# Kernel optimization log

Measured on AMD Instinct MI355X. Metric: run time of the kernel, lower is better.

The kernel has to match this reference:

```python
import jax, jax.numpy as jnp
import numpy as np

B, S, H, F, E, K = 2, 2048, 1024, 4096, 8, 2
NH = H // 128  # heads of dim 128, per SimpleMoEBlock.__init__
DH = H // NH


def _layernorm(x, g, b, eps=1e-5):
    m = x.mean(-1, keepdims=True)
    v = ((x - m) ** 2).mean(-1, keepdims=True)
    return (x - m) / jnp.sqrt(v + eps) * g + b


def _forward(x, ln_attn_g, ln_attn_b, ln_mlp_g, ln_mlp_b,
             in_proj_w, in_proj_b, out_proj_w, out_proj_b,
             router_w, fc1_w, fc1_b, fc2_w, fc2_b):
    # --- self attention (nn.MultiheadAttention, batch_first, no mask) ---
    xa = _layernorm(x, ln_attn_g, ln_attn_b)                    # [B,S,H]
    qkv = xa @ in_proj_w.T + in_proj_b                          # [B,S,3H]
    q, k, v = jnp.split(qkv, 3, axis=-1)
    def heads(t):
        return t.reshape(B, S, NH, DH).transpose(0, 2, 1, 3)    # [B,NH,S,DH]
    q, k, v = heads(q), heads(k), heads(v)
    scores = jnp.einsum('bhqd,bhkd->bhqk', q, k) / jnp.sqrt(jnp.asarray(DH, x.dtype))
    attn = jnp.einsum('bhqk,bhkd->bhqd', jax.nn.softmax(scores, axis=-1), v)
    attn = attn.transpose(0, 2, 1, 3).reshape(B, S, H)
    attn = attn @ out_proj_w.T + out_proj_b
    h = x + attn                                                # residual

    # --- MoE feed-forward ---
    y = _layernorm(h, ln_mlp_g, ln_mlp_b).reshape(B * S, H)     # flat tokens [T,H]
    logits = y @ router_w.T                                     # [T,E]
    probs = jax.nn.softmax(logits, axis=-1)
    top_scores, top_idx = jax.lax.top_k(probs, K)               # [T,K]
    # per-token per-expert combine weight; 0 for unrouted tokens -> identical
    # math to torch's index_select/index_add dispatch
    w = (jax.nn.one_hot(top_idx, E, dtype=y.dtype) * top_scores[..., None]).sum(axis=1)  # [T,E]

    combined = jnp.zeros_like(y)
    for e in range(E):  # fixed small expert count
        he = jax.nn.silu(y @ fc1_w[e].T + fc1_b[e])             # [T,F]
        oe = he @ fc2_w[e].T + fc2_b[e]                         # [T,H]
        combined = combined + oe * w[:, e:e + 1]
    return h + combined.reshape(B, S, H)


def setup_inputs() -> dict:
    key = jax.random.key(0)
    ks = jax.random.split(key, 8)
    s = 0.02
    return {
        'x': jax.random.normal(ks[0], (B, S, H), jnp.float32),
        'ln_attn_g': jnp.ones((H,), jnp.float32),
        'ln_attn_b': jnp.zeros((H,), jnp.float32),
        'ln_mlp_g': jnp.ones((H,), jnp.float32),
        'ln_mlp_b': jnp.zeros((H,), jnp.float32),
        'in_proj_w': jax.random.normal(ks[1], (3 * H, H), jnp.float32) * s,
        'in_proj_b': jnp.zeros((3 * H,), jnp.float32),
        'out_proj_w': jax.random.normal(ks[2], (H, H), jnp.float32) * s,
        'out_proj_b': jnp.zeros((H,), jnp.float32),
        'router_w': jax.random.normal(ks[3], (E, H), jnp.float32) * s,
        'fc1_w': jax.random.normal(ks[4], (E, F, H), jnp.float32) * s,
        'fc1_b': jnp.zeros((E, F), jnp.float32),
        'fc2_w': jax.random.normal(ks[5], (E, H, F), jnp.float32) * s,
        'fc2_b': jnp.zeros((E, H), jnp.float32),
    }


def reference(x, ln_attn_g, ln_attn_b, ln_mlp_g, ln_mlp_b,
              in_proj_w, in_proj_b, out_proj_w, out_proj_b,
              router_w, fc1_w, fc1_b, fc2_w, fc2_b):
    return _forward(x, ln_attn_g, ln_attn_b, ln_mlp_g, ln_mlp_b,
                    in_proj_w, in_proj_b, out_proj_w, out_proj_b,
                    router_w, fc1_w, fc1_b, fc2_w, fc2_b)
```

## Files before the change

### kernel.cpp

```cpp
#include <hip/hip_runtime.h>

#define T_TOK 4096
#define S_SEQ 2048
#define H_DIM 1024
#define H3    3072
#define NHEAD 8
#define DHEAD 128
#define F_DIM 4096
#define NEXP  8
#define MAX_RB 72
#define NSLOT 9216

typedef __bf16 bf16x8 __attribute__((ext_vector_type(8)));
typedef float  f32x4  __attribute__((ext_vector_type(4)));
typedef __attribute__((address_space(1))) const unsigned int* gas1_t;
typedef __attribute__((address_space(3))) unsigned int* las3_t;

__device__ __forceinline__ unsigned short f2bf(float f){
  unsigned int u = __builtin_bit_cast(unsigned int, f);
  u += 0x7fffu + ((u>>16)&1u);
  return (unsigned short)(u>>16);
}
__device__ __forceinline__ float bf2f(unsigned short h){
  unsigned int u = ((unsigned int)h)<<16;
  return __builtin_bit_cast(float, u);
}
__device__ __forceinline__ f32x4 MF(bf16x8 a, bf16x8 b, f32x4 c){
  return __builtin_amdgcn_mfma_f32_16x16x32_bf16(a,b,c,0,0,0);
}
__device__ __forceinline__ void gload16(const void* g, void* l){
  __builtin_amdgcn_global_load_lds((gas1_t)g, (las3_t)l, 16, 0, 0);
}
__device__ __forceinline__ float blockReduceSum(float v){
  __shared__ float sh_red[4];
  #pragma unroll
  for(int o=32;o>0;o>>=1) v += __shfl_down(v,o,64);
  int w = threadIdx.x>>6;
  if((threadIdx.x&63)==0) sh_red[w]=v;
  __syncthreads();
  float tot = sh_red[0]+sh_red[1]+sh_red[2]+sh_red[3];
  __syncthreads();
  return tot;
}

__global__ __launch_bounds__(256) void k_ln_split(const float* __restrict__ x,
    const float* __restrict__ g, const float* __restrict__ bta,
    unsigned short* __restrict__ hi, unsigned short* __restrict__ lo){
  int t = blockIdx.x, tid = threadIdx.x;
  float4 v = reinterpret_cast<const float4*>(x + (size_t)t*H_DIM)[tid];
  float mean = blockReduceSum(v.x+v.y+v.z+v.w) * (1.0f/H_DIM);
  float d0=v.x-mean,d1=v.y-mean,d2=v.z-mean,d3=v.w-mean;
  float var = blockReduceSum(d0*d0+d1*d1+d2*d2+d3*d3) * (1.0f/H_DIM);
  float rstd = rsqrtf(var + 1e-5f);
  float4 gv = reinterpret_cast<const float4*>(g)[tid];
  float4 bv = reinterpret_cast<const float4*>(bta)[tid];
  float o0=d0*rstd*gv.x+bv.x, o1=d1*rstd*gv.y+bv.y, o2=d2*rstd*gv.z+bv.z, o3=d3*rstd*gv.w+bv.w;
  size_t base = (size_t)t*H_DIM + tid*4;
  unsigned short h0=f2bf(o0),h1=f2bf(o1),h2=f2bf(o2),h3=f2bf(o3);
  *reinterpret_cast<ushort4*>(hi+base) = make_ushort4(h0,h1,h2,h3);
  *reinterpret_cast<ushort4*>(lo+base) = make_ushort4(
      f2bf(o0-bf2f(h0)), f2bf(o1-bf2f(h1)), f2bf(o2-bf2f(h2)), f2bf(o3-bf2f(h3)));
}

__global__ __launch_bounds__(256) void k_wsplit(const float* __restrict__ w,
    unsigned short* __restrict__ hi, unsigned short* __restrict__ lo, int n4){
  int i = blockIdx.x*256 + threadIdx.x;
  if(i>=n4) return;
  float4 v = reinterpret_cast<const float4*>(w)[i];
  size_t base = (size_t)i*4;
  unsigned short h0=f2bf(v.x),h1=f2bf(v.y),h2=f2bf(v.z),h3=f2bf(v.w);
  *reinterpret_cast<ushort4*>(hi+base) = make_ushort4(h0,h1,h2,h3);
  *reinterpret_cast<ushort4*>(lo+base) = make_ushort4(
      f2bf(v.x-bf2f(h0)), f2bf(v.y-bf2f(h1)), f2bf(v.z-bf2f(h2)), f2bf(v.w-bf2f(h3)));
}

__global__ __launch_bounds__(256) void k_wconv(const float* __restrict__ w,
    unsigned short* __restrict__ hi, int n4){
  int i = blockIdx.x*256 + threadIdx.x;
  if(i>=n4) return;
  float4 v = reinterpret_cast<const float4*>(w)[i];
  *reinterpret_cast<ushort4*>(hi + (size_t)i*4) =
      make_ushort4(f2bf(v.x), f2bf(v.y), f2bf(v.z), f2bf(v.w));
}

template<int EPI>
__global__ __launch_bounds__(256) void k_gemm_split(
    const unsigned short* __restrict__ Ah, const unsigned short* __restrict__ Al,
    const unsigned short* __restrict__ Bh, const unsigned short* __restrict__ Bl,
    const float* __restrict__ bias, const float* __restrict__ resid,
    unsigned short* __restrict__ Chi, unsigned short* __restrict__ Clo,
    float* __restrict__ Cf, int N, int Kd){
  int m0 = blockIdx.y*128, n0 = blockIdx.x*128;
  int tid=threadIdx.x, wid=tid>>6, lane=tid&63, lr=lane&15, lg=lane>>4;
  int wr=wid>>1, wc=wid&1;
  __shared__ unsigned short tAh[4096], tAl[4096], tBh[4096], tBl[4096];
  f32x4 acc[4][4] = {};
  for(int k0=0;k0<Kd;k0+=32){
    #pragma unroll
    for(int i=0;i<2;i++){
      int p = i*256 + tid;
      int row = p>>2, pc = p&3;
      int lc = pc ^ ((row>>1)&3);
      size_t go = (size_t)row*Kd + k0 + lc*8;
      int lb = (i*256 + wid*64)*8;
      gload16(Ah + (size_t)m0*Kd + go, tAh + lb);
      gload16(Al + (size_t)m0*Kd + go, tAl + lb);
      gload16(Bh + (size_t)n0*Kd + go, tBh + lb);
      gload16(Bl + (size_t)n0*Kd + go, tBl + lb);
    }
    asm volatile("s_waitcnt vmcnt(0)" ::: "memory");
    __syncthreads();
    bf16x8 ah[4], al[4], bh[4], bl[4];
    #pragma unroll
    for(int q=0;q<4;q++){
      int ra = wr*64+q*16+lr;
      int ia = ra*32 + ((lg ^ ((ra>>1)&3))<<3);
      ah[q] = *reinterpret_cast<const bf16x8*>(&tAh[ia]);
      al[q] = *reinterpret_cast<const bf16x8*>(&tAl[ia]);
      int rb = wc*64+q*16+lr;
      int ib = rb*32 + ((lg ^ ((rb>>1)&3))<<3);
      bh[q] = *reinterpret_cast<const bf16x8*>(&tBh[ib]);
      bl[q] = *reinterpret_cast<const bf16x8*>(&tBl[ib]);
    }
    #pragma unroll
    for(int mf=0;mf<4;mf++)
      #pragma unroll
      for(int nf=0;nf<4;nf++){
        acc[mf][nf] = MF(ah[mf], bh[nf], acc[mf][nf]);
        acc[mf][nf] = MF(ah[mf], bl[nf], acc[mf][nf]);
        acc[mf][nf] = MF(al[mf], bh[nf], acc[mf][nf]);
      }
    __syncthreads();
  }
  #pragma unroll
  for(int mf=0;mf<4;mf++)
    #pragma unroll
    for(int nf=0;nf<4;nf++)
      #pragma unroll
      for(int r=0;r<4;r++){
        int row = m0 + wr*64 + mf*16 + lg*4 + r;
        int col = n0 + wc*64 + nf*16 + lr;
        float v = acc[mf][nf][r] + bias[col];
        size_t idx = (size_t)row*N + col;
        if(EPI==0){
          unsigned short hb = f2bf(v);
          Chi[idx]=hb; Clo[idx]=f2bf(v-bf2f(hb));
        } else {
          Cf[idx] = v + resid[idx];
        }
      }
}

__global__ __launch_bounds__(256) void k_vtrans(const unsigned short* __restrict__ qh,
    const unsigned short* __restrict__ ql,
    unsigned short* __restrict__ vth, unsigned short* __restrict__ vtl){
  int bh = blockIdx.z, d0 = blockIdx.y*32, s0 = blockIdx.x*32;
  int b = bh>>3, hh = bh&7;
  int tid=threadIdx.x;
  __shared__ unsigned short th[32][40], tl[32][40];
  int sr = tid>>3, dc = (tid&7)*4;
  size_t src = ((size_t)(b*S_SEQ + s0 + sr))*H3 + 2*H_DIM + hh*DHEAD + d0 + dc;
  *reinterpret_cast<ushort4*>(&th[sr][dc]) = *reinterpret_cast<const ushort4*>(qh+src);
  *reinterpret_cast<ushort4*>(&tl[sr][dc]) = *reinterpret_cast<const ushort4*>(ql+src);
  __syncthreads();
  int dr = tid>>3, sc = (tid&7)*4;
  size_t dst = ((size_t)(bh*DHEAD) + d0+dr)*S_SEQ + s0 + sc;
  *reinterpret_cast<ushort4*>(vth+dst) = make_ushort4(th[sc][dr],th[sc+1][dr],th[sc+2][dr],th[sc+3][dr]);
  *reinterpret_cast<ushort4*>(vtl+dst) = make_ushort4(tl[sc][dr],tl[sc+1][dr],tl[sc+2][dr],tl[sc+3][dr]);
}

__global__ __launch_bounds__(256,2) void k_attn(const unsigned short* __restrict__ qkv_hi,
    const unsigned short* __restrict__ qkv_lo,
    const unsigned short* __restrict__ vt_hi, const unsigned short* __restrict__ vt_lo,
    float* __restrict__ opb, float* __restrict__ mlb, int kv_span){
  const float SCALE = 0.08838834764831843f;
  int qb = blockIdx.x, bh = blockIdx.y, zz = blockIdx.z;
  int b = bh>>3, hh = bh&7;
  int kvbase = zz*kv_span, kvend = kvbase + kv_span;
  int tid=threadIdx.x, wid=tid>>6, lane=tid&63, lr=lane&15, lg=lane>>4;
  __shared__ unsigned short kh[4096], kl[4096], vh[4096], vl[4096];
  __shared__ unsigned short ph[4][1024], pl[4][1024];
  int row0 = qb*128 + wid*32;
  bf16x8 qh_[2][4], ql_[2][4];
  #pragma unroll
  for(int j=0;j<2;j++){
    size_t qbase = ((size_t)(b*S_SEQ) + row0 + j*16 + lr)*H3 + hh*DHEAD;
    #pragma unroll
    for(int kk=0;kk<4;kk++){
      qh_[j][kk] = *reinterpret_cast<const bf16x8*>(qkv_hi + qbase + kk*32 + lg*8);
      ql_[j][kk] = *reinterpret_cast<const bf16x8*>(qkv_lo + qbase + kk*32 + lg*8);
    }
  }
  f32x4 o_acc[2][8] = {};
  float mrun[2] = {-1e30f,-1e30f};
  float lrun[2] = {0.f,0.f};

  auto STAGE = [&](int kv0){
    #pragma unroll
    for(int i=0;i<2;i++){
      int p = i*256 + tid;
      int lb = (i*256 + wid*64)*8;
      {
        int krow = p>>4, pc = p&15;
        int lc = (pc&8)|((pc&7)^(krow&7));
        size_t go = ((size_t)(b*S_SEQ + kv0 + krow))*H3 + H_DIM + hh*DHEAD + lc*8;
        gload16(qkv_hi + go, &kh[lb]);
        gload16(qkv_lo + go, &kl[lb]);
      }
      {
        int vrow = p>>2, pc = p&3;
        int lc = pc ^ ((vrow>>1)&3);
        size_t gv = ((size_t)(bh*DHEAD) + vrow)*S_SEQ + kv0 + lc*8;
        gload16(vt_hi + gv, &vh[lb]);
        gload16(vt_lo + gv, &vl[lb]);
      }
    }
  };

  for(int kv0=kvbase; kv0<kvend; kv0+=32){
    STAGE(kv0);
    asm volatile("s_waitcnt vmcnt(0)" ::: "memory");
    __syncthreads();
    f32x4 s0[2] = {}, s1[2] = {};
    __builtin_amdgcn_s_setprio(1);
    #pragma unroll
    for(int kk=0;kk<4;kk++){
      int c = kk*4+lg;
      int phys = (c&8)|((c&7)^(lr&7));
      bf16x8 kah = *reinterpret_cast<const bf16x8*>(&kh[lr*128 + phys*8]);
      bf16x8 kal = *reinterpret_cast<const bf16x8*>(&kl[lr*128 + phys*8]);
      bf16x8 kbh = *reinterpret_cast<const bf16x8*>(&kh[(16+lr)*128 + phys*8]);
      bf16x8 kbl = *reinterpret_cast<const bf16x8*>(&kl[(16+lr)*128 + phys*8]);
      #pragma unroll
      for(int j=0;j<2;j++){
        s0[j] = MF(kah, qh_[j][kk], s0[j]);
        s0[j] = MF(kah, ql_[j][kk], s0[j]);
        s0[j] = MF(kal, qh_[j][kk], s0[j]);
        s1[j] = MF(kbh, qh_[j][kk], s1[j]);
        s1[j] = MF(kbh, ql_[j][kk], s1[j]);
        s1[j] = MF(kbl, qh_[j][kk], s1[j]);
      }
    }
    __builtin_amdgcn_s_setprio(0);
    float sc[2][8]; float mt[2];
    #pragma unroll
    for(int j=0;j<2;j++){
      #pragma unroll
      for(int r=0;r<4;r++){ sc[j][r] = s0[j][r]*SCALE; sc[j][4+r] = s1[j][r]*SCALE; }
      float m_ = fmaxf(fmaxf(fmaxf(sc[j][0],sc[j][1]),fmaxf(sc[j][2],sc[j][3])),
                       fmaxf(fmaxf(sc[j][4],sc[j][5]),fmaxf(sc[j][6],sc[j][7])));
      m_ = fmaxf(m_, __shfl_xor(m_,16,64));
      m_ = fmaxf(m_, __shfl_xor(m_,32,64));
      mt[j] = m_;
    }
    int skip = __all((mt[0] <= mrun[0]+8.0f) && (mt[1] <= mrun[1]+8.0f));
    if(!skip){
      #pragma unroll
      for(int j=0;j<2;j++){
        float mn = fmaxf(mrun[j], mt[j]);
        float rs = __expf(mrun[j]-mn);
        lrun[j] *= rs; mrun[j] = mn;
        #pragma unroll
        for(int nf2=0;nf2<8;nf2++){
          f32x4 t = o_acc[j][nf2];
          t[0]*=rs; t[1]*=rs; t[2]*=rs; t[3]*=rs;
          o_acc[j][nf2] = t;
        }
      }
    }
    #pragma unroll
    for(int j=0;j<2;j++){
      float ssum = 0.f;
      #pragma unroll
      for(int i=0;i<8;i++){ sc[j][i] = __expf(sc[j][i]-mrun[j]); ssum += sc[j][i]; }
      ssum += __shfl_xor(ssum,16,64);
      ssum += __shfl_xor(ssum,32,64);
      lrun[j] += ssum;
      unsigned short hbk[8], lbk[8];
      #pragma unroll
      for(int i=0;i<8;i++){ hbk[i]=f2bf(sc[j][i]); lbk[i]=f2bf(sc[j][i]-bf2f(hbk[i])); }
      int half = (lg&1)*4;
      int a0 = j*512 + lr*32 + (((lg>>1)^(lr&3))<<3) + half;
      int a1 = j*512 + lr*32 + ((((lg>>1)+2)^(lr&3))<<3) + half;
      *reinterpret_cast<ushort4*>(&ph[wid][a0]) = make_ushort4(hbk[0],hbk[1],hbk[2],hbk[3]);
      *reinterpret_cast<ushort4*>(&pl[wid][a0]) = make_ushort4(lbk[0],lbk[1],lbk[2],lbk[3]);
      *reinterpret_cast<ushort4*>(&ph[wid][a1]) = make_ushort4(hbk[4],hbk[5],hbk[6],hbk[7]);
      *reinterpret_cast<ushort4*>(&pl[wid][a1]) = make_ushort4(lbk[4],lbk[5],lbk[6],lbk[7]);
    }
    bf16x8 pbh[2], pbl[2];
    #pragma unroll
    for(int j=0;j<2;j++){
      int pp = (lg^(lr&3))<<3;
      pbh[j] = *reinterpret_cast<const bf16x8*>(&ph[wid][j*512 + lr*32 + pp]);
      pbl[j] = *reinterpret_cast<const bf16x8*>(&pl[wid][j*512 + lr*32 + pp]);
    }
    __builtin_amdgcn_s_setprio(1);
    #pragma unroll
    for(int nf2=0;nf2<8;nf2++){
      int d = nf2*16 + lr;
      int vp = (lg ^ ((d>>1)&3))<<3;
      bf16x8 vah = *reinterpret_cast<const bf16x8*>(&vh[d*32 + vp]);
      bf16x8 val = *reinterpret_cast<const bf16x8*>(&vl[d*32 + vp]);
      #pragma unroll
      for(int j=0;j<2;j++){
        o_acc[j][nf2] = MF(vah, pbh[j], o_acc[j][nf2]);
        o_acc[j][nf2] = MF(vah, pbl[j], o_acc[j][nf2]);
        o_acc[j][nf2] = MF(val, pbh[j], o_acc[j][nf2]);
      }
    }
    __builtin_amdgcn_s_setprio(0);
    __syncthreads();
  }
  #pragma unroll
  for(int j=0;j<2;j++){
    int srow = row0 + j*16 + lr;
    size_t obase = (((size_t)zz*16 + bh)*S_SEQ + srow)*(size_t)DHEAD;
    #pragma unroll
    for(int nf2=0;nf2<8;nf2++){
      *reinterpret_cast<f32x4*>(&opb[obase + nf2*16 + lg*4]) = o_acc[j][nf2];
    }
    if(lg==0){
      *reinterpret_cast<float2*>(&mlb[(((size_t)zz*16 + bh)*S_SEQ + srow)*2]) =
          make_float2(mrun[j], lrun[j]);
    }
  }
}

__global__ __launch_bounds__(256) void k_amerge(const float* __restrict__ opb,
    const float* __restrict__ mlb, int nz,
    unsigned short* __restrict__ o_hi, unsigned short* __restrict__ o_lo){
  int bh = blockIdx.y, b = bh>>3, hh = bh&7;
  int r = threadIdx.x>>4;
  int c = (threadIdx.x&15)*8;
  int srow = blockIdx.x*16 + r;
  float mz[2], lz[2];
  float m = -1e30f;
  for(int z=0;z<nz;z++){
    const float* mlp = mlb + (((size_t)z*16 + bh)*S_SEQ + srow)*2;
    mz[z]=mlp[0]; lz[z]=mlp[1];
    m = fmaxf(m, mz[z]);
  }
  float L = 0.f, w[2];
  for(int z=0;z<nz;z++){ w[z] = __expf(mz[z]-m); L += lz[z]*w[z]; }
  float linv = 1.0f/L;
  float acc[8] = {0,0,0,0,0,0,0,0};
  for(int z=0;z<nz;z++){
    const float* o = opb + (((size_t)z*16 + bh)*S_SEQ + srow)*(size_t)DHEAD + c;
    float4 a = *reinterpret_cast<const float4*>(o);
    float4 bq = *reinterpret_cast<const float4*>(o+4);
    acc[0]+=a.x*w[z]; acc[1]+=a.y*w[z]; acc[2]+=a.z*w[z]; acc[3]+=a.w*w[z];
    acc[4]+=bq.x*w[z]; acc[5]+=bq.y*w[z]; acc[6]+=bq.z*w[z]; acc[7]+=bq.w*w[z];
  }
  size_t idx = ((size_t)(b*S_SEQ)+srow)*H_DIM + hh*DHEAD + c;
  unsigned short hp[8], lp[8];
  #pragma unroll
  for(int i=0;i<8;i++){
    float v = acc[i]*linv;
    hp[i]=f2bf(v); lp[i]=f2bf(v-bf2f(hp[i]));
  }
  *reinterpret_cast<ushort4*>(o_hi+idx)   = make_ushort4(hp[0],hp[1],hp[2],hp[3]);
  *reinterpret_cast<ushort4*>(o_hi+idx+4) = make_ushort4(hp[4],hp[5],hp[6],hp[7]);
  *reinterpret_cast<ushort4*>(o_lo+idx)   = make_ushort4(lp[0],lp[1],lp[2],lp[3]);
  *reinterpret_cast<ushort4*>(o_lo+idx+4) = make_ushort4(lp[4],lp[5],lp[6],lp[7]);
}

__global__ __launch_bounds__(256) void k_ln2_router(const float* __restrict__ h,
    const float* __restrict__ g, const float* __restrict__ bt, const float* __restrict__ rw,
    unsigned short* __restrict__ ybf, int* __restrict__ route_e, float* __restrict__ route_w){
  int t = blockIdx.x, tid = threadIdx.x;
  float4 v = reinterpret_cast<const float4*>(h + (size_t)t*H_DIM)[tid];
  float mean = blockReduceSum(v.x+v.y+v.z+v.w) * (1.0f/H_DIM);
  float d0=v.x-mean,d1=v.y-mean,d2=v.z-mean,d3=v.w-mean;
  float var = blockReduceSum(d0*d0+d1*d1+d2*d2+d3*d3) * (1.0f/H_DIM);
  float rstd = rsqrtf(var + 1e-5f);
  float4 gv = reinterpret_cast<const float4*>(g)[tid];
  float4 bv = reinterpret_cast<const float4*>(bt)[tid];
  float o0=d0*rstd*gv.x+bv.x, o1=d1*rstd*gv.y+bv.y, o2=d2*rstd*gv.z+bv.z, o3=d3*rstd*gv.w+bv.w;
  size_t base = (size_t)t*H_DIM + tid*4;
  *reinterpret_cast<ushort4*>(ybf+base) = make_ushort4(f2bf(o0),f2bf(o1),f2bf(o2),f2bf(o3));
  float part[8];
  #pragma unroll
  for(int e=0;e<8;e++){
    float4 r = reinterpret_cast<const float4*>(rw + e*H_DIM)[tid];
    part[e] = o0*r.x + o1*r.y + o2*r.z + o3*r.w;
  }
  __shared__ float sm[32];
  #pragma unroll
  for(int e=0;e<8;e++){
    float p = part[e];
    #pragma unroll
    for(int o=32;o>0;o>>=1) p += __shfl_down(p,o,64);
    if((tid&63)==0) sm[(tid>>6)*8+e] = p;
  }
  __syncthreads();
  if(tid==0){
    float lgt[8];
    #pragma unroll
    for(int e=0;e<8;e++) lgt[e] = sm[e]+sm[8+e]+sm[16+e]+sm[24+e];
    float mx = lgt[0];
    #pragma unroll
    for(int e=1;e<8;e++) mx = fmaxf(mx, lgt[e]);
    float ex[8], ssum=0.f;
    #pragma unroll
    for(int e=0;e<8;e++){ ex[e]=__expf(lgt[e]-mx); ssum+=ex[e]; }
    float inv = 1.0f/ssum;
    int e0=0; float p0=ex[0];
    for(int e=1;e<8;e++) if(ex[e]>p0){p0=ex[e];e0=e;}
    int e1=-1; float p1=-1.0f;
    for(int e=0;e<8;e++) if(e!=e0 && ex[e]>p1){p1=ex[e];e1=e;}
    route_e[2*t]=e0; route_e[2*t+1]=e1;
    route_w[2*t]=p0*inv; route_w[2*t+1]=p1*inv;
  }
}

__global__ __launch_bounds__(256) void k_compact(const int* __restrict__ route_e,
    const float* __restrict__ route_w, int* __restrict__ tok_of_slot,
    float* __restrict__ w_of_slot, int* __restrict__ slot_of_tok,
    int* __restrict__ rb_expert, int* __restrict__ rb_base){
  __shared__ int cnt[8], off[8], pos[8];
  int tid = threadIdx.x;
  if(tid<8){ cnt[tid]=0; pos[tid]=0; }
  __syncthreads();
  for(int t=tid;t<T_TOK;t+=256){
    atomicAdd(&cnt[route_e[2*t]],1);
    atomicAdd(&cnt[route_e[2*t+1]],1);
  }
  __syncthreads();
  if(tid==0){
    int o=0;
    for(int e=0;e<8;e++){ off[e]=o; o += ((cnt[e]+127)>>7)<<7; }
    int rb=0;
    for(int e=0;e<8;e++){
      int nrb = (cnt[e]+127)>>7;
      for(int r=0;r<nrb;r++){ rb_expert[rb]=e; rb_base[rb]=off[e]+r*128; rb++; }
    }
    for(;rb<MAX_RB;rb++){ rb_expert[rb]=-1; rb_base[rb]=0; }
  }
  __syncthreads();
  for(int s=tid;s<NSLOT;s+=256){ tok_of_slot[s]=0; w_of_slot[s]=0.0f; }
  __syncthreads();
  for(int t=tid;t<T_TOK;t+=256){
    int e0=route_e[2*t], e1=route_e[2*t+1];
    int s0 = off[e0] + atomicAdd(&pos[e0],1);
    tok_of_slot[s0]=t; w_of_slot[s0]=route_w[2*t]; slot_of_tok[2*t]=s0;
    int s1 = off[e1] + atomicAdd(&pos[e1],1);
    tok_of_slot[s1]=t; w_of_slot[s1]=route_w[2*t+1]; slot_of_tok[2*t+1]=s1;
  }
}

template<bool FC1, bool PRE>
__global__ __launch_bounds__(256) void k_fc(const unsigned short* __restrict__ Abuf,
    const float* __restrict__ W, const unsigned short* __restrict__ Wbf,
    const float* __restrict__ bias,
    const int* __restrict__ rb_expert, const int* __restrict__ rb_base,
    const int* __restrict__ tok_of_slot, const float* __restrict__ w_of_slot,
    unsigned short* __restrict__ he_out, float* __restrict__ oew_out){
  int rb = blockIdx.y;
  int e = rb_expert[rb];
  if(e<0) return;
  int base = rb_base[rb];
  int n0 = blockIdx.x*128;
  const int Kd = FC1 ? H_DIM : F_DIM;
  const int Nd = FC1 ? F_DIM : H_DIM;
  int tid=threadIdx.x, wid=tid>>6, lane=tid&63, lr=lane&15, lg=lane>>4;
  int wr=wid>>1, wc=wid&1;
  __shared__ unsigned short tA[4096], tB[4096];
  size_t arow_src[2];
  #pragma unroll
  for(int i=0;i<2;i++){
    int row = i*64 + (tid>>2);
    if(FC1){ int tok = tok_of_slot[base+row]; arow_src[i] = (size_t)tok*H_DIM; }
    else   { arow_src[i] = (size_t)(base+row)*F_DIM; }
  }
  const float* Wp = W + (size_t)e*F_DIM*H_DIM;
  const unsigned short* Wbp = Wbf + (size_t)e*F_DIM*H_DIM;
  f32x4 acc[4][4] = {};
  if(PRE){
    auto STAGE = [&](int k0){
      #pragma unroll
      for(int i=0;i<2;i++){
        int p = i*256+tid; int row=p>>2, pc=p&3;
        int lc = pc ^ ((row>>1)&3);
        int lb = (i*256+wid*64)*8;
        gload16(Abuf + arow_src[i] + k0 + lc*8, tA + lb);
        gload16(Wbp + (size_t)(n0+row)*Kd + k0 + lc*8, tB + lb);
      }
    };
    STAGE(0);
    asm volatile("s_waitcnt vmcnt(0)" ::: "memory");
    __syncthreads();
    for(int k0=0;k0<Kd;k0+=32){
      bf16x8 af[4], bfr[4];
      #pragma unroll
      for(int q=0;q<4;q++){
        int ra = wr*64+q*16+lr;
        af[q] = *reinterpret_cast<const bf16x8*>(&tA[ra*32 + ((lg ^ ((ra>>1)&3))<<3)]);
        int rbw = wc*64+q*16+lr;
        bfr[q] = *reinterpret_cast<const bf16x8*>(&tB[rbw*32 + ((lg ^ ((rbw>>1)&3))<<3)]);
      }
      asm volatile("s_waitcnt lgkmcnt(0)" ::: "memory");
      __builtin_amdgcn_sched_barrier(0);
      __syncthreads();
      if(k0+32 < Kd) STAGE(k0+32);
      #pragma unroll
      for(int mf=0;mf<4;mf++)
        #pragma unroll
        for(int nf=0;nf<4;nf++)
          acc[mf][nf] = MF(af[mf], bfr[nf], acc[mf][nf]);
      asm volatile("s_waitcnt vmcnt(0)" ::: "memory");
      __syncthreads();
    }
  } else {
    for(int k0=0;k0<Kd;k0+=32){
      #pragma unroll
      for(int i=0;i<2;i++){
        int p = i*256+tid; int row=p>>2, pc=p&3;
        int lc = pc ^ ((row>>1)&3);
        gload16(Abuf + arow_src[i] + k0 + lc*8, tA + (i*256+wid*64)*8);
      }
      #pragma unroll
      for(int j=0;j<4;j++){
        int f = tid*16 + j*4; int row=f>>5; int kin=f&31;
        float4 wv = *reinterpret_cast<const float4*>(Wp + (size_t)(n0+row)*Kd + k0 + kin);
        int c16 = kin>>3, half=(kin>>2)&1;
        int phys = c16 ^ ((row>>1)&3);
        *reinterpret_cast<ushort4*>(&tB[row*32 + phys*8 + half*4]) =
            make_ushort4(f2bf(wv.x), f2bf(wv.y), f2bf(wv.z), f2bf(wv.w));
      }
      asm volatile("s_waitcnt vmcnt(0)" ::: "memory");
      __syncthreads();
      bf16x8 af[4], bfr[4];
      #pragma unroll
      for(int q=0;q<4;q++){
        int ra = wr*64+q*16+lr;
        af[q] = *reinterpret_cast<const bf16x8*>(&tA[ra*32 + ((lg ^ ((ra>>1)&3))<<3)]);
        int rbw = wc*64+q*16+lr;
        bfr[q] = *reinterpret_cast<const bf16x8*>(&tB[rbw*32 + ((lg ^ ((rbw>>1)&3))<<3)]);
      }
      #pragma unroll
      for(int mf=0;mf<4;mf++)
        #pragma unroll
        for(int nf=0;nf<4;nf++)
          acc[mf][nf] = MF(af[mf], bfr[nf], acc[mf][nf]);
      __syncthreads();
    }
  }
  #pragma unroll
  for(int mf=0;mf<4;mf++)
    #pragma unroll
    for(int nf=0;nf<4;nf++)
      #pragma unroll
      for(int r=0;r<4;r++){
        int lrow = wr*64+mf*16+lg*4+r;
        int col = n0 + wc*64+nf*16+lr;
        float v = acc[mf][nf][r] + bias[(size_t)e*Nd + col];
        if(FC1){
          float sv = v/(1.0f+__expf(-v));
          he_out[(size_t)(base+lrow)*F_DIM + col] = f2bf(sv);
        } else {
          oew_out[(size_t)(base+lrow)*H_DIM + col] = w_of_slot[base+lrow]*v;
        }
      }
}

__global__ __launch_bounds__(256) void k_combine(const float* __restrict__ h,
    const float* __restrict__ oew, const int* __restrict__ slot_of_tok,
    float* __restrict__ out){
  int t = blockIdx.x, tid=threadIdx.x;
  int s0 = slot_of_tok[2*t], s1 = slot_of_tok[2*t+1];
  float4 hv = reinterpret_cast<const float4*>(h + (size_t)t*H_DIM)[tid];
  float4 a = reinterpret_cast<const float4*>(oew + (size_t)s0*H_DIM)[tid];
  float4 b = reinterpret_cast<const float4*>(oew + (size_t)s1*H_DIM)[tid];
  float4 o = make_float4(hv.x+a.x+b.x, hv.y+a.y+b.y, hv.z+a.z+b.z, hv.w+a.w+b.w);
  reinterpret_cast<float4*>(out + (size_t)t*H_DIM)[tid] = o;
}

extern "C" void kernel_launch(void* const* d_in, const int* in_sizes, int n_in,
                              void* d_out, int out_size, void* d_ws, size_t ws_size,
                              hipStream_t stream){
  const float* x    = (const float*)d_in[0];
  const float* ln1g = (const float*)d_in[1];
  const float* ln1b = (const float*)d_in[2];
  const float* ln2g = (const float*)d_in[3];
  const float* ln2b = (const float*)d_in[4];
  const float* wqkv = (const float*)d_in[5];
  const float* bqkv = (const float*)d_in[6];
  const float* wout = (const float*)d_in[7];
  const float* bout = (const float*)d_in[8];
  const float* rw   = (const float*)d_in[9];
  const float* fc1w = (const float*)d_in[10];
  const float* fc1b = (const float*)d_in[11];
  const float* fc2w = (const float*)d_in[12];
  const float* fc2b = (const float*)d_in[13];
  char* ws = (char*)d_ws;

  size_t off_ = 0;
  auto AL = [&](size_t bytes){ size_t r = off_; off_ = (off_ + bytes + 255) & ~(size_t)255; return r; };
  size_t o_xa_hi = AL((size_t)T_TOK*H_DIM*2), o_xa_lo = AL((size_t)T_TOK*H_DIM*2);
  size_t o_wq_hi = AL((size_t)H3*H_DIM*2),    o_wq_lo = AL((size_t)H3*H_DIM*2);
  size_t o_wo_hi = AL((size_t)H_DIM*H_DIM*2), o_wo_lo = AL((size_t)H_DIM*H_DIM*2);
  size_t o_qk_hi = AL((size_t)T_TOK*H3*2),    o_qk_lo = AL((size_t)T_TOK*H3*2);
  size_t o_vt_hi = AL((size_t)16*DHEAD*S_SEQ*2), o_vt_lo = AL((size_t)16*DHEAD*S_SEQ*2);
  size_t o_at_hi = AL((size_t)T_TOK*H_DIM*2), o_at_lo = AL((size_t)T_TOK*H_DIM*2);
  size_t o_he  = 0;
  size_t o_oew = (size_t)NSLOT*F_DIM*2;
  size_t o_h   = AL((size_t)T_TOK*H_DIM*4);
  size_t o_ybf = AL((size_t)T_TOK*H_DIM*2);
  size_t o_re  = AL((size_t)T_TOK*2*4);
  size_t o_rwt = AL((size_t)T_TOK*2*4);
  size_t o_st  = AL((size_t)T_TOK*2*4);
  size_t o_ts  = AL((size_t)NSLOT*4);
  size_t o_wsl = AL((size_t)NSLOT*4);
  size_t o_rbe = AL(4096);
  size_t o_rbb = AL(4096);
  size_t o_wb  = AL((size_t)NEXP*F_DIM*H_DIM*2);
  bool pre = (off_ <= ws_size);
  size_t o_op  = AL((size_t)2*16*S_SEQ*DHEAD*4 + (size_t)2*16*S_SEQ*2*4 + 256);
  bool pre2 = (off_ <= ws_size);
  (void)in_sizes; (void)n_in; (void)out_size;

  unsigned short* xa_hi = (unsigned short*)(ws+o_xa_hi);
  unsigned short* xa_lo = (unsigned short*)(ws+o_xa_lo);
  unsigned short* wq_hi = (unsigned short*)(ws+o_wq_hi);
  unsigned short* wq_lo = (unsigned short*)(ws+o_wq_lo);
  unsigned short* wo_hi = (unsigned short*)(ws+o_wo_hi);
  unsigned short* wo_lo = (unsigned short*)(ws+o_wo_lo);
  unsigned short* qk_hi = (unsigned short*)(ws+o_qk_hi);
  unsigned short* qk_lo = (unsigned short*)(ws+o_qk_lo);
  unsigned short* vt_hi = (unsigned short*)(ws+o_vt_hi);
  unsigned short* vt_lo = (unsigned short*)(ws+o_vt_lo);
  unsigned short* at_hi = (unsigned short*)(ws+o_at_hi);
  unsigned short* at_lo = (unsigned short*)(ws+o_at_lo);
  unsigned short* he    = (unsigned short*)(ws+o_he);
  float* oew   = (float*)(ws+o_oew);
  float* hbuf  = (float*)(ws+o_h);
  unsigned short* ybf = (unsigned short*)(ws+o_ybf);
  int*   route_e = (int*)(ws+o_re);
  float* route_w = (float*)(ws+o_rwt);
  int*   slot_of_tok = (int*)(ws+o_st);
  int*   tok_of_slot = (int*)(ws+o_ts);
  float* w_of_slot   = (float*)(ws+o_wsl);
  int*   rb_expert   = (int*)(ws+o_rbe);
  int*   rb_base     = (int*)(ws+o_rbb);
  unsigned short* wb = (unsigned short*)(ws+o_wb);

  int nz = pre2 ? 2 : 1;
  float* opb = pre2 ? (float*)(ws+o_op) : (float*)(ws+o_xa_hi);
  float* mlb = opb + (size_t)nz*16*S_SEQ*DHEAD;

  k_ln_split<<<T_TOK, 256, 0, stream>>>(x, ln1g, ln1b, xa_hi, xa_lo);
  k_wsplit<<<(H3*H_DIM/4+255)/256, 256, 0, stream>>>(wqkv, wq_hi, wq_lo, H3*H_DIM/4);
  k_wsplit<<<(H_DIM*H_DIM/4+255)/256, 256, 0, stream>>>(wout, wo_hi, wo_lo, H_DIM*H_DIM/4);
  k_gemm_split<0><<<dim3(H3/128, T_TOK/128), 256, 0, stream>>>(
      xa_hi, xa_lo, wq_hi, wq_lo, bqkv, nullptr, qk_hi, qk_lo, nullptr, H3, H_DIM);
  k_vtrans<<<dim3(S_SEQ/32, DHEAD/32, 16), 256, 0, stream>>>(qk_hi, qk_lo, vt_hi, vt_lo);
  k_attn<<<dim3(S_SEQ/128, 16, nz), 256, 0, stream>>>(qk_hi, qk_lo, vt_hi, vt_lo,
                                                      opb, mlb, S_SEQ/nz);
  k_amerge<<<dim3(S_SEQ/16, 16), 256, 0, stream>>>(opb, mlb, nz, at_hi, at_lo);
  k_gemm_split<1><<<dim3(H_DIM/128, T_TOK/128), 256, 0, stream>>>(
      at_hi, at_lo, wo_hi, wo_lo, bout, x, nullptr, nullptr, hbuf, H_DIM, H_DIM);
  k_ln2_router<<<T_TOK, 256, 0, stream>>>(hbuf, ln2g, ln2b, rw, ybf, route_e, route_w);
  k_compact<<<1, 256, 0, stream>>>(route_e, route_w, tok_of_slot, w_of_slot,
                                   slot_of_tok, rb_expert, rb_base);
  const int WN4 = NEXP*F_DIM*H_DIM/4;
  if(pre){
    k_wconv<<<(WN4+255)/256, 256, 0, stream>>>(fc1w, wb, WN4);
    k_fc<true,true><<<dim3(F_DIM/128, MAX_RB), 256, 0, stream>>>(
        ybf, fc1w, wb, fc1b, rb_expert, rb_base, tok_of_slot, nullptr, he, nullptr);
    k_wconv<<<(WN4+255)/256, 256, 0, stream>>>(fc2w, wb, WN4);
    k_fc<false,true><<<dim3(H_DIM/128, MAX_RB), 256, 0, stream>>>(
        he, fc2w, wb, fc2b, rb_expert, rb_base, tok_of_slot, w_of_slot, nullptr, oew);
  } else {
    k_fc<true,false><<<dim3(F_DIM/128, MAX_RB), 256, 0, stream>>>(
        ybf, fc1w, wb, fc1b, rb_expert, rb_base, tok_of_slot, nullptr, he, nullptr);
    k_fc<false,false><<<dim3(H_DIM/128, MAX_RB), 256, 0, stream>>>(
        he, fc2w, wb, fc2b, rb_expert, rb_base, tok_of_slot, w_of_slot, nullptr, oew);
  }
  k_combine<<<T_TOK, 256, 0, stream>>>(hbuf, oew, slot_of_tok, (float*)d_out);
}
```

Baseline: 755.7 us.

## Widen MoE FC GEMM K-tile to 64 and drop setprio in attention

The pre-converted bf16 expert GEMM path now stages 64-wide K tiles (doubled LDS) with an 8-way XOR swizzle and runs two MFMA sub-steps per load, instead of a software-prefetched 32-wide double-step. This halves the barrier and wait count per K but removes the overlap of global loads with compute, since loads are now issued and waited on before each compute phase. Separately, the s_setprio raises around the attention MFMA loops are removed.

```diff
diff --git a/kernel.cpp b/kernel.cpp
--- a/kernel.cpp
+++ b/kernel.cpp
@@ -222,7 +222,6 @@
     asm volatile("s_waitcnt vmcnt(0)" ::: "memory");
     __syncthreads();
     f32x4 s0[2] = {}, s1[2] = {};
-    __builtin_amdgcn_s_setprio(1);
     #pragma unroll
     for(int kk=0;kk<4;kk++){
       int c = kk*4+lg;
@@ -241,7 +240,6 @@
         s1[j] = MF(kbl, qh_[j][kk], s1[j]);
       }
     }
-    __builtin_amdgcn_s_setprio(0);
     float sc[2][8]; float mt[2];
     #pragma unroll
     for(int j=0;j<2;j++){
@@ -294,7 +292,6 @@
       pbh[j] = *reinterpret_cast<const bf16x8*>(&ph[wid][j*512 + lr*32 + pp]);
       pbl[j] = *reinterpret_cast<const bf16x8*>(&pl[wid][j*512 + lr*32 + pp]);
     }
-    __builtin_amdgcn_s_setprio(1);
     #pragma unroll
     for(int nf2=0;nf2<8;nf2++){
       int d = nf2*16 + lr;
@@ -308,7 +305,6 @@
         o_acc[j][nf2] = MF(val, pbh[j], o_acc[j][nf2]);
       }
     }
-    __builtin_amdgcn_s_setprio(0);
     __syncthreads();
   }
   #pragma unroll
@@ -464,53 +460,55 @@
   const int Nd = FC1 ? F_DIM : H_DIM;
   int tid=threadIdx.x, wid=tid>>6, lane=tid&63, lr=lane&15, lg=lane>>4;
   int wr=wid>>1, wc=wid&1;
-  __shared__ unsigned short tA[4096], tB[4096];
-  size_t arow_src[2];
-  #pragma unroll
-  for(int i=0;i<2;i++){
-    int row = i*64 + (tid>>2);
-    if(FC1){ int tok = tok_of_slot[base+row]; arow_src[i] = (size_t)tok*H_DIM; }
-    else   { arow_src[i] = (size_t)(base+row)*F_DIM; }
-  }
+  __shared__ unsigned short tA[8192], tB[8192];
   const float* Wp = W + (size_t)e*F_DIM*H_DIM;
   const unsigned short* Wbp = Wbf + (size_t)e*F_DIM*H_DIM;
   f32x4 acc[4][4] = {};
   if(PRE){
-    auto STAGE = [&](int k0){
-      #pragma unroll
-      for(int i=0;i<2;i++){
-        int p = i*256+tid; int row=p>>2, pc=p&3;
-        int lc = pc ^ ((row>>1)&3);
+    size_t arow_src[4];
+    #pragma unroll
+    for(int i=0;i<4;i++){
+      int row = i*32 + (tid>>3);
+      if(FC1){ int tok = tok_of_slot[base+row]; arow_src[i] = (size_t)tok*H_DIM; }
+      else   { arow_src[i] = (size_t)(base+row)*F_DIM; }
+    }
+    for(int k0=0;k0<Kd;k0+=64){
+      #pragma unroll
+      for(int i=0;i<4;i++){
+        int p = i*256+tid; int row=p>>3, pc=p&7;
+        int phys = pc ^ (row&7);
         int lb = (i*256+wid*64)*8;
-        gload16(Abuf + arow_src[i] + k0 + lc*8, tA + lb);
-        gload16(Wbp + (size_t)(n0+row)*Kd + k0 + lc*8, tB + lb);
-      }
-    };
-    STAGE(0);
-    asm volatile("s_waitcnt vmcnt(0)" ::: "memory");
-    __syncthreads();
-    for(int k0=0;k0<Kd;k0+=32){
-      bf16x8 af[4], bfr[4];
-      #pragma unroll
-      for(int q=0;q<4;q++){
-        int ra = wr*64+q*16+lr;
-        af[q] = *reinterpret_cast<const bf16x8*>(&tA[ra*32 + ((lg ^ ((ra>>1)&3))<<3)]);
-        int rbw = wc*64+q*16+lr;
-        bfr[q] = *reinterpret_cast<const bf16x8*>(&tB[rbw*32 + ((lg ^ ((rbw>>1)&3))<<3)]);
-      }
-      asm volatile("s_waitcnt lgkmcnt(0)" ::: "memory");
-      __builtin_amdgcn_sched_barrier(0);
-      __syncthreads();
-      if(k0+32 < Kd) STAGE(k0+32);
-      #pragma unroll
-      for(int mf=0;mf<4;mf++)
-        #pragma unroll
-        for(int nf=0;nf<4;nf++)
-          acc[mf][nf] = MF(af[mf], bfr[nf], acc[mf][nf]);
+        gload16(Abuf + arow_src[i] + k0 + phys*8, tA + lb);
+        gload16(Wbp + (size_t)(n0+row)*Kd + k0 + phys*8, tB + lb);
+      }
       asm volatile("s_waitcnt vmcnt(0)" ::: "memory");
       __syncthreads();
+      #pragma unroll
+      for(int s=0;s<2;s++){
+        bf16x8 af[4], bfr[4];
+        #pragma unroll
+        for(int q=0;q<4;q++){
+          int ra = wr*64+q*16+lr;
+          af[q] = *reinterpret_cast<const bf16x8*>(&tA[ra*64 + (((s*4+lg)^(ra&7))<<3)]);
+          int rbw = wc*64+q*16+lr;
+          bfr[q] = *reinterpret_cast<const bf16x8*>(&tB[rbw*64 + (((s*4+lg)^(rbw&7))<<3)]);
+        }
+        #pragma unroll
+        for(int mf=0;mf<4;mf++)
+          #pragma unroll
+          for(int nf=0;nf<4;nf++)
+            acc[mf][nf] = MF(af[mf], bfr[nf], acc[mf][nf]);
+      }
+      __syncthreads();
     }
   } else {
+    size_t arow_src[2];
+    #pragma unroll
+    for(int i=0;i<2;i++){
+      int row = i*64 + (tid>>2);
+      if(FC1){ int tok = tok_of_slot[base+row]; arow_src[i] = (size_t)tok*H_DIM; }
+      else   { arow_src[i] = (size_t)(base+row)*F_DIM; }
+    }
     for(int k0=0;k0<Kd;k0+=32){
       #pragma unroll
       for(int i=0;i<2;i++){
```

Measured after the change: 702.1 us. -7.1%, faster.
